# Performance work log

Hardware: AMD Instinct MI355X
Metric: run time of the kernel (lower is better)

## Reference

```python
import jax, jax.numpy as jnp
import numpy as np

BAND_WIDTH = 0.05
EPS = 1e-5
NORM_EPS = 1e-12  # F.normalize clamp_min


def _l2_normalize_channels(x):
    # x: (B, C, D, H, W); normalize over channel dim=1 like F.normalize(p=2, dim=1)
    n = jnp.sqrt(jnp.sum(x * x, axis=1, keepdims=True))
    return x / jnp.maximum(n, NORM_EPS)


def setup_inputs() -> dict:
    key = jax.random.key(0)
    k1, k2, k3 = jax.random.split(key, 3)
    B, C, D, H, W = 2, 256, 8, 8, 8
    P, K = 128, 512  # n_patches iterations, k=512 sampled voxels per patch
    S = D * H * W  # 512 spatial voxels
    t2_feat = jax.random.normal(k1, (B, C, D, H, W), dtype=jnp.float32)
    t1_feat = jax.random.normal(k2, (B, C, D, H, W), dtype=jnp.float32)
    idx = jax.random.randint(k3, (P, K), 0, S, dtype=jnp.int32)
    return {"t2_feat": t2_feat, "t1_feat": t1_feat, "idx": idx}


def reference(t2_feat, t1_feat, idx):
    B, C = t2_feat.shape[:2]
    # normalize channels, flatten spatial dims: (B, C, S)
    t2 = _l2_normalize_channels(t2_feat).reshape(B, C, -1)
    t1 = _l2_normalize_channels(t1_feat).reshape(B, C, -1)
    # gather the same random voxels for both modalities: (B, C, P, K)
    t2p = t2[:, :, idx]
    t1p = t1[:, :, idx]
    # batched cosine similarity: bmm(t2p^T, t1p) per patch -> (P, B, K, K)
    cs = jnp.einsum('bcpk,bcpl->pbkl', t2p, t1p)
    e = jnp.exp(cs / BAND_WIDTH)
    pos = jnp.diagonal(e, axis1=2, axis2=3)  # (P, B, K) exp of positives
    # InfoNCE over columns (torch dim=1 of (B,K,K)) and rows (dim=2)
    info_nce1 = pos / jnp.sum(e, axis=2)
    info_nce2 = pos / jnp.sum(e, axis=3)
    info_nce = 0.5 * (info_nce1 + info_nce2)
    # per-patch mean of -log, then mean over patches == global mean
    return jnp.mean(-jnp.log(info_nce + EPS))
```

## Files before the change

kernel.cpp:

```cpp
#include <hip/hip_runtime.h>

typedef __attribute__((ext_vector_type(8))) short bf16x8;
typedef __attribute__((ext_vector_type(4))) float f32x4;
typedef __attribute__((ext_vector_type(4))) ushort u16x4;

#define C_DIM 256
#define S_DIM 512
#define P_DIM 128
#define K_DIM 512
#define INV_BW 20.0f
#define EPS_LOSS 1e-5f

#define OFF_DIAG   0
#define OFF_EBF    1024
#define OFF_ETBF   263168
#define OFF_D1     525312
#define OFF_D2     656384
#define OFF_PART   787456
#define OFF_BAR    787584

__device__ inline ushort f2bf(float f) {
  union { float f; uint u; } v; v.f = f;
  return (ushort)((v.u + 0x7FFF + ((v.u >> 16) & 1)) >> 16);
}
__device__ inline float bf2f(ushort u) {
  union { uint u; float f; } v; v.u = ((uint)u) << 16;
  return v.f;
}

__global__ __launch_bounds__(256) void gram_exp_kernel(
    const float* __restrict__ t2, const float* __restrict__ t1,
    ushort* __restrict__ Ebf, ushort* __restrict__ ETbf,
    float* __restrict__ diag, int* __restrict__ bar) {
  __shared__ ushort A_[32][264];
  __shared__ ushort B_[32][264];
  __shared__ float sA[32], sB[32];
  int blk = blockIdx.x, tid = threadIdx.x;
  if (blk == 0 && tid == 0) bar[0] = 0;
  int mb = blk & 15, nb = (blk >> 4) & 15, b = blk >> 8;
  int m0 = mb * 32, c0 = nb * 32;
  {
    const float* pa = t2 + (b * C_DIM + tid) * S_DIM + m0;
    const float* pb = t1 + (b * C_DIM + tid) * S_DIM + c0;
    #pragma unroll
    for (int q = 0; q < 8; ++q) {
      float4 va = *reinterpret_cast<const float4*>(pa + q * 4);
      float4 vb = *reinterpret_cast<const float4*>(pb + q * 4);
      A_[q * 4 + 0][tid] = f2bf(va.x); A_[q * 4 + 1][tid] = f2bf(va.y);
      A_[q * 4 + 2][tid] = f2bf(va.z); A_[q * 4 + 3][tid] = f2bf(va.w);
      B_[q * 4 + 0][tid] = f2bf(vb.x); B_[q * 4 + 1][tid] = f2bf(vb.y);
      B_[q * 4 + 2][tid] = f2bf(vb.z); B_[q * 4 + 3][tid] = f2bf(vb.w);
    }
  }
  __syncthreads();
  if (tid < 64) {
    const ushort* row = (tid < 32) ? &A_[tid][0] : &B_[tid - 32][0];
    float a0 = 0.f, a1 = 0.f, a2 = 0.f, a3 = 0.f;
    #pragma unroll
    for (int k = 0; k < 64; ++k) {
      u16x4 v = *reinterpret_cast<const u16x4*>(row + k * 4);
      float x0 = bf2f(v.x), x1 = bf2f(v.y), x2 = bf2f(v.z), x3 = bf2f(v.w);
      a0 += x0 * x0; a1 += x1 * x1; a2 += x2 * x2; a3 += x3 * x3;
    }
    float sc = 1.0f / fmaxf(sqrtf((a0 + a1) + (a2 + a3)), 1e-12f);
    if (tid < 32) sA[tid] = sc; else sB[tid - 32] = sc;
  }
  __syncthreads();
  int wave = tid >> 6, lane = tid & 63;
  int tm = wave & 1, tn = wave >> 1;
  int lr = lane & 15, lo = lane >> 4;
  f32x4 acc = {0.f, 0.f, 0.f, 0.f};
  #pragma unroll
  for (int k = 0; k < 8; ++k) {
    bf16x8 af = *reinterpret_cast<const bf16x8*>(&A_[tm * 16 + lr][lo * 8 + k * 32]);
    bf16x8 bv = *reinterpret_cast<const bf16x8*>(&B_[tn * 16 + lr][lo * 8 + k * 32]);
    acc = __builtin_amdgcn_mfma_f32_16x16x32_bf16(af, bv, acc, 0, 0, 0);
  }
  int mg0 = m0 + tm * 16, cg0 = c0 + tn * 16;
  float bs = sB[tn * 16 + lr];
  ushort* Eb  = Ebf  + b * (S_DIM * S_DIM);
  ushort* ETb = ETbf + b * (S_DIM * S_DIM);
  float e[4]; ushort eb[4];
  #pragma unroll
  for (int r = 0; r < 4; ++r) {
    int rl = tm * 16 + lo * 4 + r;
    float ev = __expf(acc[r] * sA[rl] * bs * INV_BW);
    e[r] = ev; eb[r] = f2bf(ev);
    Eb[(m0 + rl) * S_DIM + cg0 + lr] = eb[r];
  }
  u16x4 pk = {eb[0], eb[1], eb[2], eb[3]};
  *reinterpret_cast<u16x4*>(&ETb[(cg0 + lr) * S_DIM + mg0 + lo * 4]) = pk;
  if (mg0 == cg0 && (lr >> 2) == lo) diag[b * S_DIM + mg0 + lr] = e[lr & 3];
}

__global__ __launch_bounds__(256) void denom_kernel(
    const ushort* __restrict__ Ebf, const ushort* __restrict__ ETbf,
    const int* __restrict__ idx,
    float* __restrict__ D1, float* __restrict__ D2) {
  __shared__ int hist[16][516];
  __shared__ ushort cb[16][520];
  int blk = blockIdx.x, tid = threadIdx.x;
  int m = blk & 7, ng = (blk >> 3) & 7, b = (blk >> 6) & 1, z = blk >> 7;
  int p0 = m * 16;
  #pragma unroll
  for (int i = 0; i < 32; ++i) hist[(tid * 32 + i) >> 9][(tid * 32 + i) & 511] = 0;
  __syncthreads();
  {
    int p = tid >> 4, l16 = tid & 15;
    const int* ip = idx + (p0 + p) * K_DIM + l16;
    #pragma unroll
    for (int j = 0; j < 32; ++j) atomicAdd(&hist[p][ip[j * 16]], 1);
  }
  __syncthreads();
  {
    int p = tid >> 4, l16 = tid & 15;
    #pragma unroll
    for (int j = 0; j < 32; ++j) {
      int col = l16 + j * 16;
      cb[p][col] = f2bf((float)hist[p][col]);
    }
  }
  __syncthreads();
  int wave = tid >> 6, lane = tid & 63;
  int lr = lane & 15, lo = lane >> 4;
  int col0 = (ng * 4 + wave) * 16;
  const ushort* Bmat = (z ? Ebf : ETbf) + b * (S_DIM * S_DIM);
  const ushort* bptr = Bmat + (col0 + lr) * S_DIM + lo * 8;
  f32x4 acc = {0.f, 0.f, 0.f, 0.f};
  #pragma unroll
  for (int k = 0; k < 16; ++k) {
    bf16x8 af = *reinterpret_cast<const bf16x8*>(&cb[lr][lo * 8 + k * 32]);
    bf16x8 bv = *reinterpret_cast<const bf16x8*>(bptr + k * 32);
    acc = __builtin_amdgcn_mfma_f32_16x16x32_bf16(af, bv, acc, 0, 0, 0);
  }
  float* Dp = z ? D2 : D1;
  #pragma unroll
  for (int r = 0; r < 4; ++r) {
    int p = p0 + lo * 4 + r;
    Dp[(p * 2 + b) * S_DIM + col0 + lr] = acc[r];
  }
}

__global__ __launch_bounds__(512) void loss_final_kernel(
    const int* __restrict__ idx, const float* __restrict__ diag,
    const float* __restrict__ D1, const float* __restrict__ D2,
    float* __restrict__ part, int* __restrict__ bar, float* __restrict__ out) {
  int p = blockIdx.x, k = threadIdx.x;
  int s = idx[p * K_DIM + k];
  float acc = 0.f;
  #pragma unroll
  for (int b = 0; b < 2; ++b) {
    float pos = diag[b * S_DIM + s];
    int o = (p * 2 + b) * S_DIM + s;
    float d1 = D1[o];
    float d2 = D2[o];
    acc += __logf(0.5f * (pos / d1 + pos / d2) + EPS_LOSS);
  }
  for (int o = 32; o; o >>= 1) acc += __shfl_down(acc, o);
  __shared__ float red[8];
  __shared__ int lastflag;
  if ((k & 63) == 0) red[k >> 6] = acc;
  __syncthreads();
  if (k == 0) {
    float tsum = 0.f;
    #pragma unroll
    for (int i = 0; i < 8; ++i) tsum += red[i];
    atomicExch(&part[p], tsum);
    __threadfence();
    int old = atomicAdd(&bar[0], 1);
    lastflag = (old == P_DIM - 1);
  }
  __syncthreads();
  if (lastflag) {
    __threadfence();
    float v = (k < P_DIM) ? atomicAdd(&part[k], 0.0f) : 0.0f;
    for (int o = 32; o; o >>= 1) v += __shfl_down(v, o);
    __shared__ float red2[8];
    if ((k & 63) == 0) red2[k >> 6] = v;
    __syncthreads();
    if (k == 0) {
      float tsum = 0.f;
      #pragma unroll
      for (int i = 0; i < 8; ++i) tsum += red2[i];
      out[0] = -tsum * (1.0f / (P_DIM * 2.0f * K_DIM));
    }
  }
}

extern "C" void kernel_launch(void* const* d_in, const int* in_sizes, int n_in,
                              void* d_out, int out_size, void* d_ws, size_t ws_size,
                              hipStream_t stream) {
  const float* t2 = (const float*)d_in[0];
  const float* t1 = (const float*)d_in[1];
  const int* idx  = (const int*)d_in[2];
  float* ws = (float*)d_ws;
  float*  diag   = ws + OFF_DIAG;
  ushort* Ebf    = (ushort*)(ws + OFF_EBF);
  ushort* ETbf   = (ushort*)(ws + OFF_ETBF);
  float*  D1     = ws + OFF_D1;
  float*  D2     = ws + OFF_D2;
  float*  part   = ws + OFF_PART;
  int*    bar    = (int*)(ws + OFF_BAR);

  gram_exp_kernel<<<512, 256, 0, stream>>>(t2, t1, Ebf, ETbf, diag, bar);
  denom_kernel<<<256, 256, 0, stream>>>(Ebf, ETbf, idx, D1, D2);
  loss_final_kernel<<<P_DIM, 512, 0, stream>>>(idx, diag, D1, D2, part, bar,
                                               (float*)d_out);
}
```

Before: 29.37 us.

## Fuse denominator GEMM and loss reduction into one kernel via shared-memory D tiles

Merges denom_kernel and loss_final_kernel into a single 64-block, 1024-thread kernel. Each block keeps its D1/D2 tile (16 patches x 128 columns, both directions) in shared memory and computes the log terms only for sampled indices that fall in its column range. This removes the global D1/D2 round trip and one kernel launch. In exchange the grid shrinks from 256 to 64 blocks, so fewer CUs are busy, and each block rebuilds the histogram redundantly across the four column quarters.

```diff
diff --git a/kernel.cpp b/kernel.cpp
--- a/kernel.cpp
+++ b/kernel.cpp
@@ -14,10 +14,8 @@
 #define OFF_DIAG   0
 #define OFF_EBF    1024
 #define OFF_ETBF   263168
-#define OFF_D1     525312
-#define OFF_D2     656384
-#define OFF_PART   787456
-#define OFF_BAR    787584
+#define OFF_PART   525312
+#define OFF_BAR    525376
 
 __device__ inline ushort f2bf(float f) {
   union { float f; uint u; } v; v.f = f;
@@ -93,96 +91,90 @@
   if (mg0 == cg0 && (lr >> 2) == lo) diag[b * S_DIM + mg0 + lr] = e[lr & 3];
 }
 
-__global__ __launch_bounds__(256) void denom_kernel(
+__global__ __launch_bounds__(1024) void denom_loss_kernel(
     const ushort* __restrict__ Ebf, const ushort* __restrict__ ETbf,
-    const int* __restrict__ idx,
-    float* __restrict__ D1, float* __restrict__ D2) {
+    const int* __restrict__ idx, const float* __restrict__ diag,
+    float* __restrict__ part, int* __restrict__ bar, float* __restrict__ out) {
   __shared__ int hist[16][516];
   __shared__ ushort cb[16][520];
+  __shared__ float D1L[16][132], D2L[16][132];
   int blk = blockIdx.x, tid = threadIdx.x;
-  int m = blk & 7, ng = (blk >> 3) & 7, b = (blk >> 6) & 1, z = blk >> 7;
+  int m = blk & 7, b = (blk >> 3) & 1, q = blk >> 4;
   int p0 = m * 16;
-  #pragma unroll
-  for (int i = 0; i < 32; ++i) hist[(tid * 32 + i) >> 9][(tid * 32 + i) & 511] = 0;
-  __syncthreads();
+  int wave = tid >> 6, lane = tid & 63;
+  int lr = lane & 15, lo = lane >> 4;
   {
-    int p = tid >> 4, l16 = tid & 15;
-    const int* ip = idx + (p0 + p) * K_DIM + l16;
+    int p = tid >> 6, l = tid & 63;
+    int* hp = &hist[p][0];
     #pragma unroll
-    for (int j = 0; j < 32; ++j) atomicAdd(&hist[p][ip[j * 16]], 1);
+    for (int j = 0; j < 8; ++j) hp[l * 8 + j] = 0;
+    __syncthreads();
+    const int* ip = idx + (p0 + p) * K_DIM + l;
+    #pragma unroll
+    for (int j = 0; j < 8; ++j) atomicAdd(&hp[ip[j * 64]], 1);
+    __syncthreads();
+    #pragma unroll
+    for (int j = 0; j < 8; ++j) {
+      int col = l * 8 + j;
+      cb[p][col] = f2bf((float)hp[col]);
+    }
   }
   __syncthreads();
   {
-    int p = tid >> 4, l16 = tid & 15;
+    int z = wave >> 3, jt = wave & 7;
+    int col0g = q * 128 + jt * 16, col0l = jt * 16;
+    const ushort* Bmat = (z ? Ebf : ETbf) + b * (S_DIM * S_DIM);
+    const ushort* bptr = Bmat + (col0g + lr) * S_DIM + lo * 8;
+    f32x4 acc = {0.f, 0.f, 0.f, 0.f};
     #pragma unroll
-    for (int j = 0; j < 32; ++j) {
-      int col = l16 + j * 16;
-      cb[p][col] = f2bf((float)hist[p][col]);
+    for (int k = 0; k < 16; ++k) {
+      bf16x8 af = *reinterpret_cast<const bf16x8*>(&cb[lr][lo * 8 + k * 32]);
+      bf16x8 bv = *reinterpret_cast<const bf16x8*>(bptr + k * 32);
+      acc = __builtin_amdgcn_mfma_f32_16x16x32_bf16(af, bv, acc, 0, 0, 0);
+    }
+    #pragma unroll
+    for (int r = 0; r < 4; ++r) {
+      int p = lo * 4 + r;
+      if (z) D2L[p][col0l + lr] = acc[r];
+      else   D1L[p][col0l + lr] = acc[r];
     }
   }
   __syncthreads();
-  int wave = tid >> 6, lane = tid & 63;
-  int lr = lane & 15, lo = lane >> 4;
-  int col0 = (ng * 4 + wave) * 16;
-  const ushort* Bmat = (z ? Ebf : ETbf) + b * (S_DIM * S_DIM);
-  const ushort* bptr = Bmat + (col0 + lr) * S_DIM + lo * 8;
-  f32x4 acc = {0.f, 0.f, 0.f, 0.f};
-  #pragma unroll
-  for (int k = 0; k < 16; ++k) {
-    bf16x8 af = *reinterpret_cast<const bf16x8*>(&cb[lr][lo * 8 + k * 32]);
-    bf16x8 bv = *reinterpret_cast<const bf16x8*>(bptr + k * 32);
-    acc = __builtin_amdgcn_mfma_f32_16x16x32_bf16(af, bv, acc, 0, 0, 0);
-  }
-  float* Dp = z ? D2 : D1;
-  #pragma unroll
-  for (int r = 0; r < 4; ++r) {
-    int p = p0 + lo * 4 + r;
-    Dp[(p * 2 + b) * S_DIM + col0 + lr] = acc[r];
-  }
-}
-
-__global__ __launch_bounds__(512) void loss_final_kernel(
-    const int* __restrict__ idx, const float* __restrict__ diag,
-    const float* __restrict__ D1, const float* __restrict__ D2,
-    float* __restrict__ part, int* __restrict__ bar, float* __restrict__ out) {
-  int p = blockIdx.x, k = threadIdx.x;
-  int s = idx[p * K_DIM + k];
-  float acc = 0.f;
-  #pragma unroll
-  for (int b = 0; b < 2; ++b) {
-    float pos = diag[b * S_DIM + s];
-    int o = (p * 2 + b) * S_DIM + s;
-    float d1 = D1[o];
-    float d2 = D2[o];
-    acc += __logf(0.5f * (pos / d1 + pos / d2) + EPS_LOSS);
-  }
-  for (int o = 32; o; o >>= 1) acc += __shfl_down(acc, o);
-  __shared__ float red[8];
-  __shared__ int lastflag;
-  if ((k & 63) == 0) red[k >> 6] = acc;
-  __syncthreads();
-  if (k == 0) {
-    float tsum = 0.f;
+  {
+    int p = tid >> 6, l = tid & 63;
+    const int* ip = idx + (p0 + p) * K_DIM + l;
+    float acc = 0.f;
     #pragma unroll
-    for (int i = 0; i < 8; ++i) tsum += red[i];
-    atomicExch(&part[p], tsum);
-    __threadfence();
-    int old = atomicAdd(&bar[0], 1);
-    lastflag = (old == P_DIM - 1);
-  }
-  __syncthreads();
-  if (lastflag) {
-    __threadfence();
-    float v = (k < P_DIM) ? atomicAdd(&part[k], 0.0f) : 0.0f;
-    for (int o = 32; o; o >>= 1) v += __shfl_down(v, o);
-    __shared__ float red2[8];
-    if ((k & 63) == 0) red2[k >> 6] = v;
+    for (int j = 0; j < 8; ++j) {
+      int s = ip[j * 64];
+      if ((s >> 7) == q) {
+        int sl = s & 127;
+        float pos = diag[b * S_DIM + s];
+        float d1 = D1L[p][sl];
+        float d2 = D2L[p][sl];
+        acc += __logf(0.5f * (pos / d1 + pos / d2) + EPS_LOSS);
+      }
+    }
+    for (int o = 32; o; o >>= 1) acc += __shfl_down(acc, o);
+    __shared__ float red[16];
+    __shared__ int lastflag;
+    if (lane == 0) red[wave] = acc;
     __syncthreads();
-    if (k == 0) {
+    if (tid == 0) {
       float tsum = 0.f;
       #pragma unroll
-      for (int i = 0; i < 8; ++i) tsum += red2[i];
-      out[0] = -tsum * (1.0f / (P_DIM * 2.0f * K_DIM));
+      for (int i = 0; i < 16; ++i) tsum += red[i];
+      atomicExch(&part[blk], tsum);
+      __threadfence();
+      int old = atomicAdd(&bar[0], 1);
+      lastflag = (old == 63);
+    }
+    __syncthreads();
+    if (lastflag && tid < 64) {
+      __threadfence();
+      float v = atomicAdd(&part[tid], 0.0f);
+      for (int o = 32; o; o >>= 1) v += __shfl_down(v, o);
+      if (tid == 0) out[0] = -v * (1.0f / (P_DIM * 2.0f * K_DIM));
     }
   }
 }
@@ -197,13 +189,10 @@
   float*  diag   = ws + OFF_DIAG;
   ushort* Ebf    = (ushort*)(ws + OFF_EBF);
   ushort* ETbf   = (ushort*)(ws + OFF_ETBF);
-  float*  D1     = ws + OFF_D1;
-  float*  D2     = ws + OFF_D2;
   float*  part   = ws + OFF_PART;
   int*    bar    = (int*)(ws + OFF_BAR);
 
   gram_exp_kernel<<<512, 256, 0, stream>>>(t2, t1, Ebf, ETbf, diag, bar);
-  denom_kernel<<<256, 256, 0, stream>>>(Ebf, ETbf, idx, D1, D2);
-  loss_final_kernel<<<P_DIM, 512, 0, stream>>>(idx, diag, D1, D2, part, bar,
-                                               (float*)d_out);
+  denom_loss_kernel<<<64, 1024, 0, stream>>>(Ebf, ETbf, idx, diag, part, bar,
+                                             (float*)d_out);
 }
```

Result: no change. 29.13 us (median of 2 runs) (-0.8%).
